# Kernel optimization log

Measured on AMD Instinct MI355X. Metric: run time of the kernel, lower is better.

Reference implementation:

```python
import jax, jax.numpy as jnp
import numpy as np

N = 50000   # nodes
E = 800000  # edges (avg degree 16)
D = 512     # dim_h
K = 128     # truncated eigenvectors
TJ = 4      # t_number = num_J + 1
S = D // TJ # single_out (== single_out_last here)
EPS = 1e-5


def setup_inputs() -> dict:
    key = jax.random.key(0)
    ks = jax.random.split(key, 16)
    w = lambda k, sh: jax.random.normal(k, sh, jnp.float32) * 0.02
    return {
        "x": jax.random.normal(ks[0], (N, D), jnp.float32),
        "edge_index": jax.random.randint(ks[1], (2, E), 0, N, jnp.int64),
        "eigenvector": jax.random.normal(ks[2], (N, K), jnp.float32) * (N ** -0.5),
        "filter_signals": jax.random.uniform(ks[3], (1, K, TJ), jnp.float32),
        # local GCNConv(dim_h, dim_h)
        "gcn_W": w(ks[4], (D, D)), "gcn_b": jnp.zeros((D,), jnp.float32),
        # Wave_Conv_arxiv stacked lin layers [t_number, D, S]
        "lin_W": w(ks[5], (TJ, D, S)), "lin_b": jnp.zeros((TJ, S), jnp.float32),
        "fusion_W": w(ks[6], (D, D)), "fusion_b": jnp.zeros((D,), jnp.float32),
        # batch norms (training-mode batch stats)
        "bn1l_g": jnp.ones((D,), jnp.float32), "bn1l_b": jnp.zeros((D,), jnp.float32),
        "bn1a_g": jnp.ones((D,), jnp.float32), "bn1a_b": jnp.zeros((D,), jnp.float32),
        "bn2_g": jnp.ones((D,), jnp.float32), "bn2_b": jnp.zeros((D,), jnp.float32),
        # feed-forward block
        "ff1_W": w(ks[7], (D, 2 * D)), "ff1_b": jnp.zeros((2 * D,), jnp.float32),
        "ff2_W": w(ks[8], (2 * D, D)), "ff2_b": jnp.zeros((D,), jnp.float32),
    }


def _batch_norm(h, g, b):
    m = h.mean(0)
    v = ((h - m) ** 2).mean(0)
    return (h - m) * jax.lax.rsqrt(v + EPS) * g + b


def _gcn_conv(x, edge_index, W, b):
    # PyG GCNConv with symmetric normalization and added self-loops.
    src, dst = edge_index[0], edge_index[1]
    xw = x @ W  # [N, D]
    deg = jax.ops.segment_sum(jnp.ones((edge_index.shape[1],), xw.dtype), dst,
                              num_segments=x.shape[0]) + 1.0  # + self-loop
    dinv = jax.lax.rsqrt(deg)
    norm = dinv[src] * dinv[dst]  # [E]
    agg = jax.ops.segment_sum(norm[:, None] * xw[src], dst, num_segments=x.shape[0])
    agg = agg + (dinv * dinv)[:, None] * xw  # self-loop message
    return agg + b


def _wave_conv_arxiv(x, evc, filter_signals, lin_W, lin_b, fusion_W, fusion_b):
    # evc: [N, K]; filter_signals: [1, K, TJ] -> sig [TJ, K]
    sig = filter_signals[0].T[:, :, None]  # [TJ, K, 1]
    ht = jnp.einsum('nd,tds->tns', x, lin_W) + lin_b[:, None, :]  # [TJ, N, S]
    u = jnp.einsum('nk,tns->tks', evc, ht) * sig                  # [TJ, K, S]
    v = jax.nn.relu(jnp.einsum('nk,tks->tns', evc, u))            # [TJ, N, S]
    u2 = jnp.einsum('nk,tns->tks', evc, v) * sig                  # [TJ, K, S]
    out = jnp.einsum('nk,tks->tns', evc, u2)                      # [TJ, N, S]
    comb = jnp.transpose(out, (1, 0, 2)).reshape(x.shape[0], -1)  # [N, D]
    return jax.nn.relu(comb @ fusion_W + fusion_b)


def reference(x, edge_index, eigenvector, filter_signals,
              gcn_W, gcn_b, lin_W, lin_b, fusion_W, fusion_b,
              bn1l_g, bn1l_b, bn1a_g, bn1a_b, bn2_g, bn2_b,
              ff1_W, ff1_b, ff2_W, ff2_b):
    h_in = x
    # local GCN branch + residual + BN
    h_local = _gcn_conv(x, edge_index, gcn_W, gcn_b)
    h_local = _batch_norm(h_in + h_local, bn1l_g, bn1l_b)
    # global WaveGC branch + residual + BN
    h_attn = _wave_conv_arxiv(x, eigenvector, filter_signals,
                              lin_W, lin_b, fusion_W, fusion_b)
    h_attn = _batch_norm(h_in + h_attn, bn1a_g, bn1a_b)
    h = h_local + h_attn
    # feed-forward block + residual + BN
    ff = jax.nn.relu(h @ ff1_W + ff1_b) @ ff2_W + ff2_b
    h = _batch_norm(h + ff, bn2_g, bn2_b)
    return h
```

## Files before the change

### kernel.cpp

```cpp
#include <hip/hip_runtime.h>
#include <hip/hip_bf16.h>

#define NN 50000
#define DD 512
#define KE 128
#define TJN 4
#define BNEPS 1e-5f
#define ZC 64
#define KPAD 50016
#define SKE 800

typedef __attribute__((ext_vector_type(8))) short short8;
typedef __attribute__((ext_vector_type(4))) float floatx4;

__device__ __forceinline__ float bf2f(unsigned short h){
  return __uint_as_float(((unsigned int)h) << 16);
}
__device__ __forceinline__ unsigned short f2bf(float f){
  unsigned int u = __float_as_uint(f);
  unsigned int r = (u + 0x7FFF + ((u >> 16) & 1)) >> 16;
  return (unsigned short)r;
}
__device__ __forceinline__ float load1(const void* p, long i, int bf){
  if (bf) return bf2f(((const unsigned short*)p)[i]);
  return ((const float*)p)[i];
}
__device__ __forceinline__ void store1(void* p, long i, int bf, float v){
  if (bf) ((unsigned short*)p)[i] = f2bf(v);
  else ((float*)p)[i] = v;
}

typedef __attribute__((address_space(3))) unsigned int lds_uint_t;
typedef __attribute__((address_space(1))) unsigned int gbl_uint_t;
__device__ __forceinline__ void gload16(const void* gp, void* lp){
  __builtin_amdgcn_global_load_lds((const gbl_uint_t*)gp, (lds_uint_t*)lp, 16, 0, 0);
}

__global__ void detect_kernel(const void* xraw, const void* eraw, int* flags){
  if (blockIdx.x == 0 && threadIdx.x == 0){
    const unsigned short* p = (const unsigned short*)xraw;
    int cnt = 0;
    for (int i = 0; i < 128; i++){
      int e = (p[i] >> 7) & 0xFF;
      if (e >= 110 && e <= 133) cnt++;
    }
    flags[0] = (cnt >= 96) ? 1 : 0;
    const unsigned int* q = (const unsigned int*)eraw;
    int z = 0;
    for (int i = 0; i < 64; i++) if (q[2*i+1] == 0u) z++;
    flags[1] = (z >= 48) ? 1 : 0;
  }
}

struct P13 { const void* p[12]; };
__global__ void cvt_params(P13 pp, float* __restrict__ dst, const int* __restrict__ flags){
  int bf = flags[0];
  int i = blockIdx.x * 256 + threadIdx.x;
  if (i >= 6656) return;
  const void* s; int off;
  if (i < 2048){ s = pp.p[i >> 9]; off = i & 511; }
  else if (i < 3072){ s = pp.p[4]; off = i - 2048; }
  else if (i < 3584){ s = pp.p[5]; off = i - 3072; }
  else { int j = (i - 3584) >> 9; s = pp.p[6 + j]; off = (i - 3584) & 511; }
  dst[i] = load1(s, off, bf);
}

__global__ __launch_bounds__(256) void cvt_bt(
    const void* __restrict__ src, unsigned short* __restrict__ dst1,
    unsigned short* __restrict__ dst2, int K, int Nc, int ldK,
    const int* __restrict__ flags){
  int bf = flags[0];
  __shared__ unsigned short T[64][66];
  int bk = blockIdx.y * 64, bc = blockIdx.x * 64;
  int tid = threadIdx.x;
#pragma unroll
  for (int p = 0; p < 16; p++){
    int idx = p * 256 + tid;
    int r = idx >> 6, c = idx & 63;
    unsigned short h = 0;
    if (bk + r < K){
      h = f2bf(load1(src, (long)(bk + r) * Nc + bc + c, bf));
      dst1[(long)(bk + r) * Nc + bc + c] = h;
    }
    T[r][c] = h;
  }
  __syncthreads();
#pragma unroll
  for (int p = 0; p < 16; p++){
    int idx = p * 256 + tid;
    int r = idx >> 6, c = idx & 63;
    if (bk + c < ldK)
      dst2[(long)(bc + r) * ldK + bk + c] = T[c][r];
  }
}

__global__ __launch_bounds__(256) void cvt_t(
    const void* __restrict__ src, unsigned short* __restrict__ dst,
    int K, int Nc, int ldK, long srcz, long dstz, int smode,
    const int* __restrict__ flags){
  int bf = (smode == 2) ? flags[0] : smode;
  __shared__ unsigned short T[64][66];
  int bk = blockIdx.y * 64, bc = blockIdx.x * 64;
  long so = (long)blockIdx.z * srcz;
  long dof = (long)blockIdx.z * dstz;
  int tid = threadIdx.x;
#pragma unroll
  for (int p = 0; p < 16; p++){
    int idx = p * 256 + tid;
    int r = idx >> 6, c = idx & 63;
    float v = 0.f;
    if (bk + r < K) v = load1(src, so + (long)(bk + r) * Nc + bc + c, bf);
    T[r][c] = f2bf(v);
  }
  __syncthreads();
#pragma unroll
  for (int p = 0; p < 16; p++){
    int idx = p * 256 + tid;
    int r = idx >> 6, c = idx & 63;
    if (bk + c < ldK)
      dst[dof + (long)(bc + r) * ldK + bk + c] = T[c][r];
  }
}

__global__ void cvt_idx(const void* __restrict__ src, int* __restrict__ dst,
                        long n, const int* __restrict__ flags){
  int w64 = flags[1];
  long i = (long)blockIdx.x * blockDim.x + threadIdx.x;
  long stride = (long)gridDim.x * blockDim.x;
  for (; i < n; i += stride)
    dst[i] = w64 ? (int)((const long long*)src)[i] : ((const int*)src)[i];
}

__global__ void deg_kernel(const int* __restrict__ dst, int* __restrict__ deg, int E){
  int i = blockIdx.x * blockDim.x + threadIdx.x;
  if (i < E) atomicAdd(&deg[dst[i]], 1);
}

__global__ __launch_bounds__(1024) void scan_kernel(const int* __restrict__ deg,
                                                    int* __restrict__ rowptr, int E){
  __shared__ int lds[1024];
  int t = threadIdx.x;
  const int CH = (NN + 1023) / 1024;
  int base = t * CH;
  int s = 0;
  for (int i = 0; i < CH; i++){
    int idx = base + i;
    if (idx < NN) s += deg[idx];
  }
  lds[t] = s;
  __syncthreads();
  for (int off = 1; off < 1024; off <<= 1){
    int v = (t >= off) ? lds[t - off] : 0;
    __syncthreads();
    lds[t] += v;
    __syncthreads();
  }
  int ex = (t == 0) ? 0 : lds[t - 1];
  for (int i = 0; i < CH; i++){
    int idx = base + i;
    if (idx < NN){ rowptr[idx] = ex; ex += deg[idx]; }
  }
  if (t == 1023) rowptr[NN] = ex;
}

__global__ void dinv_kernel(const int* __restrict__ deg, float* __restrict__ dinv){
  int i = blockIdx.x * blockDim.x + threadIdx.x;
  if (i < NN) dinv[i] = rsqrtf((float)deg[i] + 1.0f);
}

__global__ void scatter_kernel(const int* __restrict__ srcv, const int* __restrict__ dstv,
                               const int* __restrict__ rowptr, int* __restrict__ cursor,
                               int* __restrict__ csr, int E){
  int i = blockIdx.x * blockDim.x + threadIdx.x;
  if (i < E){
    int d = dstv[i];
    int pos = atomicAdd(&cursor[d], 1);
    csr[rowptr[d] + pos] = srcv[i];
  }
}

__global__ __launch_bounds__(64) void gcn_gather(
    const int* __restrict__ rowptr, const int* __restrict__ csr,
    const float* __restrict__ dinv, const void* __restrict__ xw ,
    const void* __restrict__ X, const float* __restrict__ bias,
    float* __restrict__ out, const int* __restrict__ flags){
  int d = blockIdx.x;
  int lane = threadIdx.x;
  __shared__ int s_idx[64];
  __shared__ float s_dv[64];
  int start = rowptr[d], end = rowptr[d + 1];
  float dd = dinv[d];
  float acc[8];
#pragma unroll
  for (int k = 0; k < 8; k++) acc[k] = 0.f;
  const unsigned short* xwp = (const unsigned short*)xw;
  int c0 = lane * 8;
  for (int j0 = start; j0 < end; j0 += 64){
    int cnt = min(64, end - j0);
    __syncthreads();
    if (lane < cnt){
      int s = csr[j0 + lane];
      s_idx[lane] = s;
      s_dv[lane] = dinv[s];
    }
    __syncthreads();
    for (int t = 0; t < cnt; t++){
      int s = s_idx[t];
      float nm = dd * s_dv[t];
      union { float4 f; unsigned short u[8]; } r;
      r.f = *(const float4*)(xwp + (long)s * DD + c0);
#pragma unroll
      for (int k = 0; k < 8; k++) acc[k] += nm * bf2f(r.u[k]);
    }
  }
  int xf = flags[0];
  long base = (long)d * DD + c0;
  union { float4 f; unsigned short u[8]; } sf;
  sf.f = *(const float4*)(xwp + base);
  float d2 = dd * dd;
#pragma unroll
  for (int k = 0; k < 8; k++)
    out[base + k] = load1(X, base + k, xf) + acc[k] + d2 * bf2f(sf.u[k]) + bias[c0 + k];
}

__global__ __launch_bounds__(512) void bn_stats(const float* __restrict__ T,
                                                float* __restrict__ sum,
                                                float* __restrict__ sumsq){
  int c = threadIdx.x;
  long r0 = (long)blockIdx.x * 128;
  float s = 0.f, q = 0.f;
  for (int r = 0; r < 128; r++){
    long rr = r0 + r;
    if (rr < NN){
      float v = T[rr * DD + c];
      s += v; q += v * v;
    }
  }
  atomicAdd(&sum[c], s);
  atomicAdd(&sumsq[c], q);
}

__global__ void bn_apply(const float* __restrict__ T,
                         const float* __restrict__ sum, const float* __restrict__ sumsq,
                         const float* __restrict__ g, const float* __restrict__ b,
                         const void* __restrict__ addsrc, int addmode,
                         void* __restrict__ out, int outmode,
                         unsigned short* __restrict__ out2,
                         const int* __restrict__ flags){
  int am = (addmode == 2) ? flags[0] : addmode;
  int om = (outmode == 2) ? flags[0] : outmode;
  long i = (long)blockIdx.x * blockDim.x + threadIdx.x;
  long stride = (long)gridDim.x * blockDim.x;
  long n = (long)NN * DD;
  const float invN = 1.0f / (float)NN;
  for (; i < n; i += stride){
    int c = (int)(i & 511);
    float m = sum[c] * invN;
    float var = sumsq[c] * invN - m * m;
    float v = (T[i] - m) * rsqrtf(var + BNEPS) * g[c] + b[c];
    if (addsrc) v += load1(addsrc, i, am);
    store1(out, i, om, v);
    if (out2) out2[i] = f2bf(v);
  }
}

__global__ void zero_out_bf16(void* out, long nbytes){
  long i = (long)blockIdx.x * blockDim.x + threadIdx.x;
  long stride = (long)gridDim.x * blockDim.x;
  long n = nbytes / 2;
  for (; i < n; i += stride) ((unsigned short*)out)[i] = 0;
}

__global__ __launch_bounds__(256) void gemm_mfma(
    const unsigned short* __restrict__ A, const unsigned short* __restrict__ Bt,
    void* __restrict__ C, int M, int N, int Kd, int lda, int ldc,
    const float* __restrict__ bias, const void* __restrict__ addsrc, int dorelu,
    int addmode, int cmode, const int* __restrict__ flags){
  int fl = flags[0];
  int adbf = (addmode == 2) ? fl : addmode;
  int cbf = (cmode == 2) ? fl : cmode;
  __shared__ unsigned short Asl[128 * 32];
  __shared__ unsigned short Bsl[128 * 32];
  const int tid = threadIdx.x;

  int nx = gridDim.x;
  int nwg = nx * gridDim.y;
  int p = blockIdx.y * nx + blockIdx.x;
  int q8 = nwg >> 3, r8 = nwg & 7;
  int xcd = p & 7, off = p >> 3;
  int id = (xcd < r8 ? xcd * (q8 + 1) : r8 * (q8 + 1) + (xcd - r8) * q8) + off;
  int by = id / nx, bx = id - by * nx;
  const int bm = by * 128, bn = bx * 128;

  const int lane = tid & 63, wave = tid >> 6;
  const int wm = (wave & 1) * 64, wn = (wave >> 1) * 64;
  const int q = lane >> 4, l16 = lane & 15;
  const int swz = (q ^ ((l16 >> 1) & 3)) << 3;
  floatx4 acc[4][4];
#pragma unroll
  for (int i = 0; i < 4; i++)
#pragma unroll
    for (int j = 0; j < 4; j++)
#pragma unroll
      for (int r = 0; r < 4; r++) acc[i][j][r] = 0.f;

  const int sbase = wave << 7;

  for (int k0 = 0; k0 < Kd; k0 += 32){
    __syncthreads();
#pragma unroll
    for (int pp = 0; pp < 2; pp++){
      int slot = sbase + (pp << 6) + lane;
      int row = slot >> 2;
      int ssl = (slot & 3) ^ ((slot >> 3) & 3);
      int rA = bm + row; if (rA > M - 1) rA = M - 1;
      gload16(A + (long)rA * lda + k0 + (ssl << 3), &Asl[(sbase + (pp << 6)) << 3]);
      gload16(Bt + (long)(bn + row) * Kd + k0 + (ssl << 3), &Bsl[(sbase + (pp << 6)) << 3]);
    }
    __syncthreads();
    short8 af[4], bfr[4];
#pragma unroll
    for (int i = 0; i < 4; i++){
      int ra = wm + i * 16 + l16;
      af[i] = *(const short8*)&Asl[(ra << 5) + swz];
      int rb = wn + i * 16 + l16;
      bfr[i] = *(const short8*)&Bsl[(rb << 5) + swz];
    }
#pragma unroll
    for (int i = 0; i < 4; i++)
#pragma unroll
      for (int j = 0; j < 4; j++)
        acc[i][j] = __builtin_amdgcn_mfma_f32_16x16x32_bf16(af[i], bfr[j], acc[i][j], 0, 0, 0);
  }
#pragma unroll
  for (int i = 0; i < 4; i++){
#pragma unroll
    for (int r = 0; r < 4; r++){
      int row = bm + wm + i * 16 + q * 4 + r;
      if (row >= M) continue;
#pragma unroll
      for (int j = 0; j < 4; j++){
        int col = bn + wn + j * 16 + l16;
        float v = acc[i][j][r];
        if (bias) v += bias[col];
        if (dorelu) v = fmaxf(v, 0.f);
        if (addsrc) v += load1(addsrc, (long)row * ldc + col, adbf);
        store1(C, (long)row * ldc + col, cbf, v);
      }
    }
  }
}

__global__ __launch_bounds__(256) void gemm_mfma_t(
    const unsigned short* __restrict__ A, const unsigned short* __restrict__ Bt,
    unsigned short* __restrict__ Ct, int M, int Kd, int lda, int ldct,
    const float* __restrict__ bias, int dorelu){
  __shared__ unsigned short Asl[128 * 32];
  __shared__ unsigned short Bsl[128 * 32];
  __shared__ unsigned short sc[128 * 132];
  const int tid = threadIdx.x;

  int nx = gridDim.x;
  int nwg = nx * gridDim.y;
  int p = blockIdx.y * nx + blockIdx.x;
  int q8 = nwg >> 3, r8 = nwg & 7;
  int xcd = p & 7, off = p >> 3;
  int id = (xcd < r8 ? xcd * (q8 + 1) : r8 * (q8 + 1) + (xcd - r8) * q8) + off;
  int by = id / nx, bx = id - by * nx;
  const int bm = by * 128, bn = bx * 128;

  const int lane = tid & 63, wave = tid >> 6;
  const int wm = (wave & 1) * 64, wn = (wave >> 1) * 64;
  const int q = lane >> 4, l16 = lane & 15;
  const int swz = (q ^ ((l16 >> 1) & 3)) << 3;
  floatx4 acc[4][4];
#pragma unroll
  for (int i = 0; i < 4; i++)
#pragma unroll
    for (int j = 0; j < 4; j++)
#pragma unroll
      for (int r = 0; r < 4; r++) acc[i][j][r] = 0.f;

  const int sbase = wave << 7;

  for (int k0 = 0; k0 < Kd; k0 += 32){
    __syncthreads();
#pragma unroll
    for (int pp = 0; pp < 2; pp++){
      int slot = sbase + (pp << 6) + lane;
      int row = slot >> 2;
      int ssl = (slot & 3) ^ ((slot >> 3) & 3);
      int rA = bm + row; if (rA > M - 1) rA = M - 1;
      gload16(A + (long)rA * lda + k0 + (ssl << 3), &Asl[(sbase + (pp << 6)) << 3]);
      gload16(Bt + (long)(bn + row) * Kd + k0 + (ssl << 3), &Bsl[(sbase + (pp << 6)) << 3]);
    }
    __syncthreads();
    short8 af[4], bfr[4];
#pragma unroll
    for (int i = 0; i < 4; i++){
      int ra = wm + i * 16 + l16;
      af[i] = *(const short8*)&Asl[(ra << 5) + swz];
      int rb = wn + i * 16 + l16;
      bfr[i] = *(const short8*)&Bsl[(rb << 5) + swz];
    }
#pragma unroll
    for (int i = 0; i < 4; i++)
#pragma unroll
      for (int j = 0; j < 4; j++)
        acc[i][j] = __builtin_amdgcn_mfma_f32_16x16x32_bf16(af[i], bfr[j], acc[i][j], 0, 0, 0);
  }
#pragma unroll
  for (int i = 0; i < 4; i++){
#pragma unroll
    for (int j = 0; j < 4; j++){
      int lr0 = wm + i * 16 + q * 4;
      int lc = wn + j * 16 + l16;
      float v0 = acc[i][j][0], v1 = acc[i][j][1], v2 = acc[i][j][2], v3 = acc[i][j][3];
      if (bias){ float bb = bias[bn + lc]; v0 += bb; v1 += bb; v2 += bb; v3 += bb; }
      if (dorelu){
        v0 = fmaxf(v0, 0.f); v1 = fmaxf(v1, 0.f);
        v2 = fmaxf(v2, 0.f); v3 = fmaxf(v3, 0.f);
      }
      ushort4 pk;
      pk.x = f2bf(v0); pk.y = f2bf(v1); pk.z = f2bf(v2); pk.w = f2bf(v3);
      *(ushort4*)&sc[lc * 132 + lr0] = pk;
    }
  }
  __syncthreads();
#pragma unroll
  for (int pp = 0; pp < 8; pp++){
    int idx = pp * 2048 + tid * 8;
    int r2 = idx >> 7, c2 = idx & 127;
    int gc = bm + c2;
    if (gc >= ldct) continue;
    short8 o;
#pragma unroll
    for (int e = 0; e < 8; e++)
      ((unsigned short*)&o)[e] = (gc + e < M) ? sc[r2 * 132 + c2 + e] : (unsigned short)0;
    *(short8*)&Ct[(long)(bn + r2) * ldct + gc] = o;
  }
}

__global__ __launch_bounds__(256) void gemm_sk(
    const unsigned short* __restrict__ A, const unsigned short* __restrict__ Bt,
    float* __restrict__ P, int ldk){
  __shared__ unsigned short Asl[128 * 32];
  __shared__ unsigned short Bsl[128 * 32];
  const int tid = threadIdx.x;
  const int bn = blockIdx.x * 128;
  const int ks = blockIdx.z * SKE;
  const int ke = min(ks + SKE, KPAD);

  const int lane = tid & 63, wave = tid >> 6;
  const int wm = (wave & 1) * 64, wn = (wave >> 1) * 64;
  const int q = lane >> 4, l16 = lane & 15;
  const int swz = (q ^ ((l16 >> 1) & 3)) << 3;
  floatx4 acc[4][4];
#pragma unroll
  for (int i = 0; i < 4; i++)
#pragma unroll
    for (int j = 0; j < 4; j++)
#pragma unroll
      for (int r = 0; r < 4; r++) acc[i][j][r] = 0.f;

  const int sbase = wave << 7;

  for (int k0 = ks; k0 < ke; k0 += 32){
    __syncthreads();
#pragma unroll
    for (int pp = 0; pp < 2; pp++){
      int slot = sbase + (pp << 6) + lane;
      int row = slot >> 2;
      int ssl = (slot & 3) ^ ((slot >> 3) & 3);
      gload16(A + (long)row * ldk + k0 + (ssl << 3), &Asl[(sbase + (pp << 6)) << 3]);
      gload16(Bt + (long)(bn + row) * ldk + k0 + (ssl << 3), &Bsl[(sbase + (pp << 6)) << 3]);
    }
    __syncthreads();
    short8 af[4], bfr[4];
#pragma unroll
    for (int i = 0; i < 4; i++){
      int ra = wm + i * 16 + l16;
      af[i] = *(const short8*)&Asl[(ra << 5) + swz];
      int rb = wn + i * 16 + l16;
      bfr[i] = *(const short8*)&Bsl[(rb << 5) + swz];
    }
#pragma unroll
    for (int i = 0; i < 4; i++)
#pragma unroll
      for (int j = 0; j < 4; j++)
        acc[i][j] = __builtin_amdgcn_mfma_f32_16x16x32_bf16(af[i], bfr[j], acc[i][j], 0, 0, 0);
  }
  long base = (long)blockIdx.z * (KE * DD);
#pragma unroll
  for (int i = 0; i < 4; i++){
#pragma unroll
    for (int r = 0; r < 4; r++){
      int row = wm + i * 16 + q * 4 + r;
#pragma unroll
      for (int j = 0; j < 4; j++){
        int col = bn + wn + j * 16 + l16;
        P[base + (long)row * DD + col] = acc[i][j][r];
      }
    }
  }
}

__global__ void reduce_part(const float* __restrict__ P, float* __restrict__ C){
  int i = blockIdx.x * 256 + threadIdx.x;
  float s = 0.f;
  for (int z = 0; z < ZC; z++) s += P[(long)z * (KE * DD) + i];
  C[i] = s;
}

__global__ __launch_bounds__(256) void evsum_kernel(const unsigned short* __restrict__ EVb,
                                                    float* __restrict__ evsum){
  int b = blockIdx.x, t = threadIdx.x;
  int k = t & 127, half = t >> 7;
  float s = 0.f;
  for (int r = 0; r < 128; r += 2){
    int row = b * 128 + r + half;
    if (row < NN) s += bf2f(EVb[(long)row * KE + k]);
  }
  atomicAdd(&evsum[k], s);
}

__global__ __launch_bounds__(256) void wave_mix(
    const float* __restrict__ XU, const unsigned short* __restrict__ W2t,
    const float* __restrict__ evsum, const float* __restrict__ b2,
    const float* __restrict__ filt, unsigned short* __restrict__ Ut){
  int i = blockIdx.x * 256 + threadIdx.x;
  int k = i >> 9, c = i & 511;
  float acc = evsum[k] * b2[c];
  const float* xr = XU + (long)k * DD;
  const unsigned short* wr = W2t + (long)c * DD;
#pragma unroll 4
  for (int d = 0; d < DD; d += 8){
    float4 x0 = *(const float4*)(xr + d);
    float4 x1 = *(const float4*)(xr + d + 4);
    ushort4 w0 = *(const ushort4*)(wr + d);
    ushort4 w1 = *(const ushort4*)(wr + d + 4);
    acc += x0.x * bf2f(w0.x) + x0.y * bf2f(w0.y) + x0.z * bf2f(w0.z) + x0.w * bf2f(w0.w)
         + x1.x * bf2f(w1.x) + x1.y * bf2f(w1.y) + x1.z * bf2f(w1.z) + x1.w * bf2f(w1.w);
  }
  float v = acc * filt[k * TJN + (c >> 7)];
  Ut[(long)c * KE + k] = f2bf(v);
}

__global__ __launch_bounds__(256) void mix2(
    const float* __restrict__ U2, const unsigned short* __restrict__ Wft,
    const float* __restrict__ filt, unsigned short* __restrict__ M2t){
  int i = blockIdx.x * 256 + threadIdx.x;
  int k = i & 127, j = i >> 7;
  float fs0 = filt[k * TJN + 0], fs1 = filt[k * TJN + 1];
  float fs2 = filt[k * TJN + 2], fs3 = filt[k * TJN + 3];
  const float* ur = U2 + (long)k * DD;
  const unsigned short* wr = Wft + (long)j * DD;
  float acc = 0.f;
#pragma unroll
  for (int t = 0; t < 4; t++){
    float a = 0.f;
    for (int c = t * 128; c < t * 128 + 128; c += 8){
      float4 x0 = *(const float4*)(ur + c);
      float4 x1 = *(const float4*)(ur + c + 4);
      ushort4 w0 = *(const ushort4*)(wr + c);
      ushort4 w1 = *(const ushort4*)(wr + c + 4);
      a += x0.x * bf2f(w0.x) + x0.y * bf2f(w0.y) + x0.z * bf2f(w0.z) + x0.w * bf2f(w0.w)
         + x1.x * bf2f(w1.x) + x1.y * bf2f(w1.y) + x1.z * bf2f(w1.z) + x1.w * bf2f(w1.w);
    }
    acc += (t == 0 ? fs0 : t == 1 ? fs1 : t == 2 ? fs2 : fs3) * a;
  }
  M2t[(long)j * KE + k] = f2bf(acc);
}

extern "C" void kernel_launch(void* const* d_in, const int* in_sizes, int n_in,
                              void* d_out, int out_size, void* d_ws, size_t ws_size,
                              hipStream_t stream){
  const int E = in_sizes[1] / 2;
  const long NB = (long)NN * DD;
  float* ws = (float*)d_ws;
  (void)n_in;

  size_t cur = 0;
  auto alloc = [&](size_t n){ size_t o = cur; cur += (n + 63) & ~(size_t)63; return o; };

  size_t o_flags = alloc(64);
  size_t o_zero  = cur;
  size_t o_U     = alloc((size_t)KE * DD);
  size_t o_U2    = alloc((size_t)KE * DD);
  size_t o_stats = alloc(6 * DD);
  size_t o_evsum = alloc(KE);
  size_t o_ideg  = alloc(NN);
  size_t o_cur   = alloc(NN);
  size_t zlen    = cur - o_zero;
  size_t o_dinv  = alloc(NN);
  size_t o_rowp  = alloc(NN + 64);
  size_t o_filt  = alloc(KE * TJN);
  size_t o_bgcn  = alloc(DD);
  size_t o_b2    = alloc(DD);
  size_t o_bfus  = alloc(DD);
  size_t o_bff1  = alloc(2 * DD);
  size_t o_bff2  = alloc(DD);
  size_t o_bn    = alloc(6 * DD);
  size_t o_Wgt   = alloc((size_t)DD * DD / 2);
  size_t o_W2t   = alloc((size_t)DD * DD / 2);
  size_t o_Wft   = alloc((size_t)DD * DD / 2);
  size_t o_W1t   = alloc((size_t)DD * DD);
  size_t o_Wff2t = alloc((size_t)DD * DD);
  size_t o_Ut    = alloc((size_t)KE * DD / 2);
  size_t o_M2t   = alloc((size_t)KE * DD / 2);
  size_t o_idx   = alloc((size_t)2 * E);
  size_t o_csr   = alloc((size_t)E);
  size_t o_part  = alloc((size_t)ZC * KE * DD);
  size_t o_BF    = alloc(NB);
  size_t o_BA    = alloc(NB / 2);
  size_t o_BHL   = alloc(NB / 2);
  size_t o_Xb    = alloc(NB / 2);
  size_t o_EVb   = alloc((size_t)NN * KE / 2);
  size_t o_Hb    = alloc(NB / 2);

  if (cur * 4 > ws_size){
    zero_out_bf16<<<2048, 256, 0, stream>>>(d_out, (long)out_size * 2);
    return;
  }

  int* flags = (int*)(ws + o_flags);
  float* BF  = ws + o_BF;
  void* BA   = (void*)(ws + o_BA);
  void* BHL  = (void*)(ws + o_BHL);
  void* F1   = BA;
  int* srcv  = (int*)(ws + o_idx);
  int* dstv  = srcv + E;
  int* ideg  = (int*)(ws + o_ideg);
  int* cursor= (int*)(ws + o_cur);
  int* rowp  = (int*)(ws + o_rowp);
  int* csr   = (int*)(ws + o_csr);
  float* dinv= ws + o_dinv;
  float* U   = ws + o_U;
  float* U2  = ws + o_U2;
  float* st  = ws + o_stats;
  float* Part= ws + o_part;
  unsigned short* Wgt   = (unsigned short*)(ws + o_Wgt);
  unsigned short* W2t   = (unsigned short*)(ws + o_W2t);
  unsigned short* Wft   = (unsigned short*)(ws + o_Wft);
  unsigned short* W1t   = (unsigned short*)(ws + o_W1t);
  unsigned short* Wff2t = (unsigned short*)(ws + o_Wff2t);
  unsigned short* Ut    = (unsigned short*)(ws + o_Ut);
  unsigned short* M2t   = (unsigned short*)(ws + o_M2t);
  unsigned short* Xb    = (unsigned short*)(ws + o_Xb);
  unsigned short* EVb   = (unsigned short*)(ws + o_EVb);
  unsigned short* Hb    = (unsigned short*)(ws + o_Hb);
  unsigned short* XbT  = (unsigned short*)(ws + o_BF);
  unsigned short* EVbT = (unsigned short*)(ws + o_BF + 12804160);
  unsigned short* VAt  = (unsigned short*)BA;

  detect_kernel<<<1, 64, 0, stream>>>(d_in[0], d_in[1], flags);
  hipMemsetAsync(ws + o_zero, 0, zlen * 4, stream);

  P13 pp;
  pp.p[0] = d_in[3];  pp.p[1] = d_in[5];  pp.p[2] = d_in[7];  pp.p[3] = d_in[9];
  pp.p[4] = d_in[17]; pp.p[5] = d_in[19];
  for (int i = 0; i < 6; i++) pp.p[6 + i] = d_in[10 + i];
  cvt_params<<<26, 256, 0, stream>>>(pp, ws + o_filt, flags);

  cvt_bt<<<dim3(8, 782), 256, 0, stream>>>(d_in[0], Xb,  XbT,  NN, DD, KPAD, flags);
  cvt_bt<<<dim3(2, 782), 256, 0, stream>>>(d_in[2], EVb, EVbT, NN, KE, KPAD, flags);
  cvt_t<<<dim3(8, 8),   256, 0, stream>>>(d_in[4],  Wgt,   DD, DD, DD, 0, 0, 2, flags);
  cvt_t<<<dim3(2, 8, 4),256, 0, stream>>>(d_in[6],  W2t,   DD, 128, DD,
                                          (long)DD * 128, (long)128 * DD, 2, flags);
  cvt_t<<<dim3(8, 8),   256, 0, stream>>>(d_in[8],  Wft,   DD, DD, DD, 0, 0, 2, flags);
  cvt_t<<<dim3(16, 8),  256, 0, stream>>>(d_in[16], W1t,   DD, 2 * DD, DD, 0, 0, 2, flags);
  cvt_t<<<dim3(8, 16),  256, 0, stream>>>(d_in[18], Wff2t, 2 * DD, DD, 2 * DD, 0, 0, 2, flags);
  cvt_idx<<<4096, 256, 0, stream>>>(d_in[1], srcv, 2L * E, flags);

  deg_kernel<<<(E + 255) / 256, 256, 0, stream>>>(dstv, ideg, E);
  scan_kernel<<<1, 1024, 0, stream>>>(ideg, rowp, E);
  dinv_kernel<<<(NN + 255) / 256, 256, 0, stream>>>(ideg, dinv);
  scatter_kernel<<<(E + 255) / 256, 256, 0, stream>>>(srcv, dstv, rowp, cursor, csr, E);

  const int MT = (NN + 127) / 128;
  dim3 blk(256);
  const void* Xr = d_in[0];

  gemm_sk<<<dim3(4, 1, ZC), blk, 0, stream>>>(EVbT, XbT, Part, KPAD);
  reduce_part<<<256, 256, 0, stream>>>(Part, U);
  evsum_kernel<<<MT, 256, 0, stream>>>(EVb, ws + o_evsum);
  wave_mix<<<256, 256, 0, stream>>>(U, W2t, ws + o_evsum, ws + o_b2,
                                    ws + o_filt, Ut);
  gemm_mfma_t<<<dim3(4, MT), blk, 0, stream>>>(EVb, Ut, VAt, NN, KE, KE, KPAD,
                                               nullptr, 1);
  gemm_sk<<<dim3(4, 1, ZC), blk, 0, stream>>>(EVbT, VAt, Part, KPAD);
  reduce_part<<<256, 256, 0, stream>>>(Part, U2);
  mix2<<<256, 256, 0, stream>>>(U2, Wft, ws + o_filt, M2t);
  gemm_mfma<<<dim3(4, MT), blk, 0, stream>>>(EVb, M2t, BF, NN, DD, KE, KE, DD,
                                             ws + o_bfus, Xr, 1, 2, 0, flags);
  bn_stats<<<MT, 512, 0, stream>>>(BF, st + 2 * DD, st + 3 * DD);
  bn_apply<<<4096, 256, 0, stream>>>(BF, st + 2 * DD, st + 3 * DD,
                                     ws + o_bn + 2 * DD, ws + o_bn + 3 * DD,
                                     nullptr, 0, BHL, 1, nullptr, flags);

  gemm_mfma<<<dim3(4, MT), blk, 0, stream>>>(Xb, Wgt, BA, NN, DD, DD, DD, DD,
                                             nullptr, nullptr, 0, 0, 1, flags);
  gcn_gather<<<NN, 64, 0, stream>>>(rowp, csr, dinv, BA, Xr, ws + o_bgcn, BF, flags);
  bn_stats<<<MT, 512, 0, stream>>>(BF, st + 0, st + DD);
  bn_apply<<<4096, 256, 0, stream>>>(BF, st + 0, st + DD,
                                     ws + o_bn + 0 * DD, ws + o_bn + 1 * DD,
                                     BHL, 1, BF, 0, Hb, flags);

  gemm_mfma<<<dim3(8, MT), blk, 0, stream>>>(Hb, W1t, F1, NN, 2 * DD, DD, DD, 2 * DD,
                                             ws + o_bff1, nullptr, 1, 0, 1, flags);
  gemm_mfma<<<dim3(4, MT), blk, 0, stream>>>((const unsigned short*)F1, Wff2t, BF,
                                             NN, DD, 2 * DD, 2 * DD, DD,
                                             ws + o_bff2, BF, 0, 0, 0, flags);
  bn_stats<<<MT, 512, 0, stream>>>(BF, st + 4 * DD, st + 5 * DD);
  bn_apply<<<4096, 256, 0, stream>>>(BF, st + 4 * DD, st + 5 * DD,
                                     ws + o_bn + 4 * DD, ws + o_bn + 5 * DD,
                                     nullptr, 0, d_out, 2, nullptr, flags);
}
```

Baseline: 1.742 ms.

## Stage GEMM epilogue through LDS and keep intermediates in bf16

The GEMM epilogue now writes accumulators to shared memory and then emits coalesced 16-byte row stores, with a vectorized residual add. Several fp32 intermediates (fusion output, BN1 output, FF2 output) are stored as bf16 and fed to the BN kernels through a mode flag. The FF residual now reads the bf16 Hb instead of the fp32 buffer. The aim is less HBM traffic and better-coalesced stores, at the cost of extra epilogue syncs and bf16 rounding in values that feed batch-norm statistics and residuals.

```diff
diff --git a/kernel.cpp b/kernel.cpp
--- a/kernel.cpp
+++ b/kernel.cpp
@@ -223,7 +223,7 @@
     out[base + k] = load1(X, base + k, xf) + acc[k] + d2 * bf2f(sf.u[k]) + bias[c0 + k];
 }
 
-__global__ __launch_bounds__(512) void bn_stats(const float* __restrict__ T,
+__global__ __launch_bounds__(512) void bn_stats(const void* __restrict__ T, int tmode,
                                                 float* __restrict__ sum,
                                                 float* __restrict__ sumsq){
   int c = threadIdx.x;
@@ -232,7 +232,7 @@
   for (int r = 0; r < 128; r++){
     long rr = r0 + r;
     if (rr < NN){
-      float v = T[rr * DD + c];
+      float v = load1(T, rr * DD + c, tmode);
       s += v; q += v * v;
     }
   }
@@ -240,12 +240,11 @@
   atomicAdd(&sumsq[c], q);
 }
 
-__global__ void bn_apply(const float* __restrict__ T,
+__global__ void bn_apply(const void* __restrict__ T, int tmode,
                          const float* __restrict__ sum, const float* __restrict__ sumsq,
                          const float* __restrict__ g, const float* __restrict__ b,
                          const void* __restrict__ addsrc, int addmode,
                          void* __restrict__ out, int outmode,
-                         unsigned short* __restrict__ out2,
                          const int* __restrict__ flags){
   int am = (addmode == 2) ? flags[0] : addmode;
   int om = (outmode == 2) ? flags[0] : outmode;
@@ -257,10 +256,9 @@
     int c = (int)(i & 511);
     float m = sum[c] * invN;
     float var = sumsq[c] * invN - m * m;
-    float v = (T[i] - m) * rsqrtf(var + BNEPS) * g[c] + b[c];
+    float v = (load1(T, i, tmode) - m) * rsqrtf(var + BNEPS) * g[c] + b[c];
     if (addsrc) v += load1(addsrc, i, am);
     store1(out, i, om, v);
-    if (out2) out2[i] = f2bf(v);
   }
 }
 
@@ -279,8 +277,9 @@
   int fl = flags[0];
   int adbf = (addmode == 2) ? fl : addmode;
   int cbf = (cmode == 2) ? fl : cmode;
-  __shared__ unsigned short Asl[128 * 32];
-  __shared__ unsigned short Bsl[128 * 32];
+  __shared__ unsigned short lds[8192];
+  unsigned short* Asl = lds;
+  unsigned short* Bsl = lds + 4096;
   const int tid = threadIdx.x;
 
   int nx = gridDim.x;
@@ -332,22 +331,58 @@
       for (int j = 0; j < 4; j++)
         acc[i][j] = __builtin_amdgcn_mfma_f32_16x16x32_bf16(af[i], bfr[j], acc[i][j], 0, 0, 0);
   }
-#pragma unroll
-  for (int i = 0; i < 4; i++){
-#pragma unroll
-    for (int r = 0; r < 4; r++){
-      int row = bm + wm + i * 16 + q * 4 + r;
-      if (row >= M) continue;
+  __syncthreads();
+  float* sc = (float*)lds;
+#pragma unroll
+  for (int ps = 0; ps < 8; ps++){
+    int i0 = ps & 3;
+    int wmp = (ps >> 2) * 64;
+    if (wm == wmp){
 #pragma unroll
       for (int j = 0; j < 4; j++){
-        int col = bn + wn + j * 16 + l16;
-        float v = acc[i][j][r];
-        if (bias) v += bias[col];
-        if (dorelu) v = fmaxf(v, 0.f);
-        if (addsrc) v += load1(addsrc, (long)row * ldc + col, adbf);
-        store1(C, (long)row * ldc + col, cbf, v);
+        int col = wn + j * 16 + l16;
+        float bb = bias ? bias[bn + col] : 0.f;
+#pragma unroll
+        for (int r = 0; r < 4; r++){
+          float v = acc[i0][j][r] + bb;
+          if (dorelu) v = fmaxf(v, 0.f);
+          sc[(q * 4 + r) * 132 + col] = v;
+        }
       }
     }
+    __syncthreads();
+    {
+      int rl = tid >> 4, c8 = (tid & 15) << 3;
+      int grow = bm + ps * 16 + rl;
+      if (grow < M){
+        float4 f0 = *(float4*)&sc[rl * 132 + c8];
+        float4 f1 = *(float4*)&sc[rl * 132 + c8 + 4];
+        long offc = (long)grow * ldc + bn + c8;
+        if (addsrc){
+          if (adbf){
+            ushort4 h0 = *(const ushort4*)((const unsigned short*)addsrc + offc);
+            ushort4 h1 = *(const ushort4*)((const unsigned short*)addsrc + offc + 4);
+            f0.x += bf2f(h0.x); f0.y += bf2f(h0.y); f0.z += bf2f(h0.z); f0.w += bf2f(h0.w);
+            f1.x += bf2f(h1.x); f1.y += bf2f(h1.y); f1.z += bf2f(h1.z); f1.w += bf2f(h1.w);
+          } else {
+            float4 a0 = *(const float4*)((const float*)addsrc + offc);
+            float4 a1 = *(const float4*)((const float*)addsrc + offc + 4);
+            f0.x += a0.x; f0.y += a0.y; f0.z += a0.z; f0.w += a0.w;
+            f1.x += a1.x; f1.y += a1.y; f1.z += a1.z; f1.w += a1.w;
+          }
+        }
+        if (cbf){
+          union { short8 s; unsigned short u[8]; } o;
+          o.u[0] = f2bf(f0.x); o.u[1] = f2bf(f0.y); o.u[2] = f2bf(f0.z); o.u[3] = f2bf(f0.w);
+          o.u[4] = f2bf(f1.x); o.u[5] = f2bf(f1.y); o.u[6] = f2bf(f1.z); o.u[7] = f2bf(f1.w);
+          *(short8*)((unsigned short*)C + offc) = o.s;
+        } else {
+          *(float4*)((float*)C + offc) = f0;
+          *(float4*)((float*)C + offc + 4) = f1;
+        }
+      }
+    }
+    __syncthreads();
   }
 }
 
@@ -691,28 +726,28 @@
   gemm_sk<<<dim3(4, 1, ZC), blk, 0, stream>>>(EVbT, VAt, Part, KPAD);
   reduce_part<<<256, 256, 0, stream>>>(Part, U2);
   mix2<<<256, 256, 0, stream>>>(U2, Wft, ws + o_filt, M2t);
-  gemm_mfma<<<dim3(4, MT), blk, 0, stream>>>(EVb, M2t, BF, NN, DD, KE, KE, DD,
-                                             ws + o_bfus, Xr, 1, 2, 0, flags);
-  bn_stats<<<MT, 512, 0, stream>>>(BF, st + 2 * DD, st + 3 * DD);
-  bn_apply<<<4096, 256, 0, stream>>>(BF, st + 2 * DD, st + 3 * DD,
+  gemm_mfma<<<dim3(4, MT), blk, 0, stream>>>(EVb, M2t, BA, NN, DD, KE, KE, DD,
+                                             ws + o_bfus, Xr, 1, 2, 1, flags);
+  bn_stats<<<MT, 512, 0, stream>>>(BA, 1, st + 2 * DD, st + 3 * DD);
+  bn_apply<<<4096, 256, 0, stream>>>(BA, 1, st + 2 * DD, st + 3 * DD,
                                      ws + o_bn + 2 * DD, ws + o_bn + 3 * DD,
-                                     nullptr, 0, BHL, 1, nullptr, flags);
+                                     nullptr, 0, BHL, 1, flags);
 
   gemm_mfma<<<dim3(4, MT), blk, 0, stream>>>(Xb, Wgt, BA, NN, DD, DD, DD, DD,
                                              nullptr, nullptr, 0, 0, 1, flags);
   gcn_gather<<<NN, 64, 0, stream>>>(rowp, csr, dinv, BA, Xr, ws + o_bgcn, BF, flags);
-  bn_stats<<<MT, 512, 0, stream>>>(BF, st + 0, st + DD);
-  bn_apply<<<4096, 256, 0, stream>>>(BF, st + 0, st + DD,
+  bn_stats<<<MT, 512, 0, stream>>>(BF, 0, st + 0, st + DD);
+  bn_apply<<<4096, 256, 0, stream>>>(BF, 0, st + 0, st + DD,
                                      ws + o_bn + 0 * DD, ws + o_bn + 1 * DD,
-                                     BHL, 1, BF, 0, Hb, flags);
+                                     BHL, 1, Hb, 1, flags);
 
   gemm_mfma<<<dim3(8, MT), blk, 0, stream>>>(Hb, W1t, F1, NN, 2 * DD, DD, DD, 2 * DD,
                                              ws + o_bff1, nullptr, 1, 0, 1, flags);
-  gemm_mfma<<<dim3(4, MT), blk, 0, stream>>>((const unsigned short*)F1, Wff2t, BF,
+  gemm_mfma<<<dim3(4, MT), blk, 0, stream>>>((const unsigned short*)F1, Wff2t, Xb,
                                              NN, DD, 2 * DD, 2 * DD, DD,
-                                             ws + o_bff2, BF, 0, 0, 0, flags);
-  bn_stats<<<MT, 512, 0, stream>>>(BF, st + 4 * DD, st + 5 * DD);
-  bn_apply<<<4096, 256, 0, stream>>>(BF, st + 4 * DD, st + 5 * DD,
+                                             ws + o_bff2, Hb, 0, 1, 1, flags);
+  bn_stats<<<MT, 512, 0, stream>>>(Xb, 1, st + 4 * DD, st + 5 * DD);
+  bn_apply<<<4096, 256, 0, stream>>>(Xb, 1, st + 4 * DD, st + 5 * DD,
                                      ws + o_bn + 4 * DD, ws + o_bn + 5 * DD,
-                                     nullptr, 0, d_out, 2, nullptr, flags);
-}
+                                     nullptr, 0, d_out, 2, flags);
+}
```

New measurement: 1.486 ms. 1.17x faster.
